# Kernel tuning notes

Measured on AMD Instinct MI355X. Metric: run time of the kernel, lower is better.

The kernel has to match this reference:

```python
import jax, jax.numpy as jnp
import numpy as np

# Per-type input feature dims (NODE_DIM values); max dim = 128 = padded width of x.
NODE_DIMS = np.array([16, 32, 64, 128, 64, 32, 16, 128], dtype=np.int32)
N_TYPES = 8
MAX_DIM = 128
FEAT = 256          # node_feature_dim
N_GRAPHS = 100000   # batch_size; one node of each type per graph


def setup_inputs() -> dict:
    key = jax.random.key(0)
    k1, k2, k3 = jax.random.split(key, 3)
    num_nodes = N_GRAPHS * N_TYPES
    x = jax.random.normal(k1, (num_nodes, MAX_DIM), dtype=jnp.float32)
    # Per-type Linear weights, padded to MAX_DIM on the input axis.
    W = jax.random.normal(k2, (N_TYPES, FEAT, MAX_DIM), dtype=jnp.float32) * 0.05
    b = jax.random.normal(k3, (N_TYPES, FEAT), dtype=jnp.float32) * 0.05
    return {"x": x, "W": W, "b": b}


def reference(x, W, b):
    # Node n = g*N_TYPES + k is the type-k node of graph g (the gather index
    # ptr[b] + node_name.index(k) in the original). Dropout is eval-mode (identity).
    # Mask weight columns beyond each type's true input dim: equivalent to
    # slicing x[:, :NODE_DIM[k]] before the per-type Linear.
    mask = (jnp.arange(MAX_DIM)[None, None, :] < jnp.asarray(NODE_DIMS)[:, None, None]).astype(x.dtype)  # [T,1,D]
    W_eff = W * mask  # [T,F,D]
    xg = x.reshape(N_GRAPHS, N_TYPES, MAX_DIM)  # [G,T,D]
    y = jnp.einsum("gtd,tfd->gtf", xg, W_eff) + b[None, :, :]  # [G,T,F]
    return y.reshape(N_GRAPHS * N_TYPES, FEAT)
```

## Files before the change

kernel.cpp:

```cpp
#include <hip/hip_runtime.h>

#define N_GRAPHS 100000
#define NTYPES 8
#define MAXD 128
#define FEAT 256
#define SPB 8
#define GPB (16 * SPB)

typedef __attribute__((ext_vector_type(8))) short short8;
typedef __attribute__((ext_vector_type(4))) float f32x4;
typedef __attribute__((ext_vector_type(4))) unsigned uint4v;

constexpr int KSN[NTYPES]   = {1, 1, 2, 4, 2, 1, 1, 4};
constexpr int KSOFF[NTYPES] = {0, 1, 2, 4, 8, 10, 11, 12};
constexpr int OFFC[NTYPES]  = {0, 32, 64, 128, 256, 320, 352, 384};
#define KTOT 16
#define LDA 524

__device__ __forceinline__ unsigned f2bf_u(float f) {
    unsigned u = __builtin_bit_cast(unsigned, f);
    return (u + 0x7fffu + ((u >> 16) & 1u)) >> 16;
}
__device__ __forceinline__ unsigned cvt2(float lo, float hi) {
    return f2bf_u(lo) | (f2bf_u(hi) << 16);
}
__device__ __forceinline__ short8 cvt8(f32x4 a, f32x4 b) {
    uint4v u;
    u.x = cvt2(a.x, a.y); u.y = cvt2(a.z, a.w);
    u.z = cvt2(b.x, b.y); u.w = cvt2(b.z, b.w);
    return __builtin_bit_cast(short8, u);
}

__global__ __launch_bounds__(256)
void prepack_w(const float* __restrict__ W, short8* __restrict__ wp)
{
    const int idx  = blockIdx.x * 256 + threadIdx.x;
    const int c16  = idx & 15;
    const int cgrp = (idx >> 4) & 3;
    const int ks   = (idx >> 6) & 3;
    const int ct   = (idx >> 8) & 15;
    const int t    = (idx >> 12) & 7;
    const int col  = ct * 16 + c16;
    const int k    = ks * 32 + cgrp * 8;
    const int dim  = 16 << ((0x30123210u >> (4 * t)) & 0xf);
    const float* src = W + ((size_t)t * FEAT + col) * MAXD + k;
    f32x4 a = *(const f32x4*)src;
    f32x4 b = *(const f32x4*)(src + 4);
    #pragma unroll
    for (int j = 0; j < 4; ++j) {
        if (k + j     >= dim) a[j] = 0.f;
        if (k + 4 + j >= dim) b[j] = 0.f;
    }
    wp[idx] = cvt8(a, b);
}

__device__ __forceinline__ void stage16(const float* __restrict__ x, int gs,
                                        unsigned short (* __restrict__ As)[LDA], int tid)
{
    const int row = tid >> 6;
    const int c8  = tid & 63;
    const int t = (c8 >= 4) + (c8 >= 8) + (c8 >= 16) + (c8 >= 32) +
                  (c8 >= 40) + (c8 >= 44) + (c8 >= 48);
    const int off8 = c8 < 4 ? 0 : c8 < 8 ? 4 : c8 < 16 ? 8 : c8 < 32 ? 16 :
                     c8 < 40 ? 32 : c8 < 44 ? 40 : c8 < 48 ? 44 : 48;
    const int k8 = c8 - off8;
    const float* rp = x + (((size_t)(gs + row)) * NTYPES + t) * MAXD + k8 * 8;
    f32x4 v0 = __builtin_nontemporal_load((const f32x4*)rp);
    f32x4 v1 = __builtin_nontemporal_load((const f32x4*)rp + 1);
    *(short8*)&As[row][c8 * 8] = cvt8(v0, v1);
}

template<int T, bool PRE>
__device__ __forceinline__ void load_bf(short8* __restrict__ Bf,
                                        const short8* __restrict__ wp,
                                        const float* __restrict__ W,
                                        int wave, int cgrp, int c16)
{
    if constexpr (PRE) {
        #pragma unroll
        for (int ks = 0; ks < KSN[T]; ++ks)
            Bf[KSOFF[T] + ks] = wp[(((T * 16 + wave) * 4 + ks) * 4 + cgrp) * 16 + c16];
    } else {
        constexpr int DIM = (T==0||T==6) ? 16 : (T==1||T==5) ? 32 : (T==2||T==4) ? 64 : 128;
        const int col = wave * 16 + c16;
        #pragma unroll
        for (int ks = 0; ks < KSN[T]; ++ks) {
            const int k = ks * 32 + cgrp * 8;
            const float* wf = W + ((size_t)T * FEAT + col) * MAXD + k;
            f32x4 a = *(const f32x4*)wf;
            f32x4 b = *(const f32x4*)(wf + 4);
            #pragma unroll
            for (int j = 0; j < 4; ++j) {
                if (k + j     >= DIM) a[j] = 0.f;
                if (k + 4 + j >= DIM) b[j] = 0.f;
            }
            Bf[KSOFF[T] + ks] = cvt8(a, b);
        }
    }
    if constexpr (T + 1 < NTYPES) load_bf<T + 1, PRE>(Bf, wp, W, wave, cgrp, c16);
}

template<int T>
__device__ __forceinline__ void compute_types(const short8* __restrict__ Bf,
                                              const unsigned short (* __restrict__ A)[LDA],
                                              float* __restrict__ out,
                                              const float* __restrict__ bias_g,
                                              int gs, int wave, int cgrp, int c16)
{
    f32x4 acc = {0.f, 0.f, 0.f, 0.f};
    #pragma unroll
    for (int ks = 0; ks < KSN[T]; ++ks) {
        short8 a = *(const short8*)&A[c16][OFFC[T] + ks * 32 + cgrp * 8];
        acc = __builtin_amdgcn_mfma_f32_16x16x32_bf16(a, Bf[KSOFF[T] + ks], acc, 0, 0, 0);
    }
    const int col = wave * 16 + c16;
    const float bv = bias_g[T * FEAT + col];
    #pragma unroll
    for (int r = 0; r < 4; ++r) {
        const int g = gs + cgrp * 4 + r;
        __builtin_nontemporal_store(acc[r] + bv,
            &out[((size_t)g * NTYPES + T) * FEAT + col]);
    }
    if constexpr (T + 1 < NTYPES) compute_types<T + 1>(Bf, A, out, bias_g, gs, wave, cgrp, c16);
}

template<bool PRE>
__global__ __launch_bounds__(1024, 4)
void node_enc(const float* __restrict__ x, const short8* __restrict__ wp,
              const float* __restrict__ W, const float* __restrict__ bias_g,
              float* __restrict__ out)
{
    __shared__ __align__(16) unsigned short As[2][16][LDA];
    const int tid  = threadIdx.x;
    const int lane = tid & 63;
    const int wave = tid >> 6;
    const int cgrp = lane >> 4;
    const int c16  = lane & 15;
    const int g0   = blockIdx.x * GPB;

    short8 Bf[KTOT];
    load_bf<0, PRE>(Bf, wp, W, wave, cgrp, c16);

    stage16(x, g0, As[0], tid);

    for (int s = 0; s < SPB; ++s) {
        const int gs = g0 + s * 16;
        if (gs >= N_GRAPHS) break;
        __syncthreads();
        const int gn = gs + 16;
        if (s + 1 < SPB && gn < N_GRAPHS)
            stage16(x, gn, As[(s + 1) & 1], tid);
        compute_types<0>(Bf, As[s & 1], out, bias_g, gs, wave, cgrp, c16);
    }
}

extern "C" void kernel_launch(void* const* d_in, const int* in_sizes, int n_in,
                              void* d_out, int out_size, void* d_ws, size_t ws_size,
                              hipStream_t stream)
{
    const float* x = (const float*)d_in[0];
    const float* W = (const float*)d_in[1];
    const float* b = (const float*)d_in[2];
    float* out = (float*)d_out;

    const int grid = (N_GRAPHS + GPB - 1) / GPB;
    const size_t wp_bytes = (size_t)32768 * sizeof(short8);

    if (ws_size >= wp_bytes) {
        short8* wp = (short8*)d_ws;
        prepack_w<<<128, 256, 0, stream>>>(W, wp);
        node_enc<true><<<grid, 1024, 0, stream>>>(x, wp, W, b, out);
    } else {
        node_enc<false><<<grid, 1024, 0, stream>>>(x, nullptr, W, b, out);
    }
}
```

Before: 328.0 us.

## Use persistent 256-thread blocks with 4 column tiles per wave and per-step weight reloads

Replaces the 1024-thread blocks (one 16-column tile per wave, weights held in registers across all steps) with a fixed grid of 768 blocks of 256 threads. Each block covers a contiguous range of graphs and each wave computes four 16-column tiles, which reuses each A fragment across four MFMAs. Weights and bias are now reloaded from the prepacked buffer (L2) for every type on every step instead of staying resident, and each thread stages four rows of x. A tail path with clamped loads and guarded stores handles ranges that are not multiples of 16. This trades register-resident weights for more MFMA work per A load and fewer, persistent blocks, at the cost of repeated weight loads.

```diff
diff --git a/kernel.cpp b/kernel.cpp
--- a/kernel.cpp
+++ b/kernel.cpp
@@ -4,18 +4,15 @@
 #define NTYPES 8
 #define MAXD 128
 #define FEAT 256
-#define SPB 8
-#define GPB (16 * SPB)
+#define NBLK 768
+#define LDA 524
 
 typedef __attribute__((ext_vector_type(8))) short short8;
 typedef __attribute__((ext_vector_type(4))) float f32x4;
 typedef __attribute__((ext_vector_type(4))) unsigned uint4v;
 
-constexpr int KSN[NTYPES]   = {1, 1, 2, 4, 2, 1, 1, 4};
-constexpr int KSOFF[NTYPES] = {0, 1, 2, 4, 8, 10, 11, 12};
-constexpr int OFFC[NTYPES]  = {0, 32, 64, 128, 256, 320, 352, 384};
-#define KTOT 16
-#define LDA 524
+constexpr int KSN[NTYPES]  = {1, 1, 2, 4, 2, 1, 1, 4};
+constexpr int OFFC[NTYPES] = {0, 32, 64, 128, 256, 320, 352, 384};
 
 __device__ __forceinline__ unsigned f2bf_u(float f) {
     unsigned u = __builtin_bit_cast(unsigned, f);
@@ -57,75 +54,93 @@
 __device__ __forceinline__ void stage16(const float* __restrict__ x, int gs,
                                         unsigned short (* __restrict__ As)[LDA], int tid)
 {
-    const int row = tid >> 6;
-    const int c8  = tid & 63;
+    const int c8 = tid & 63;
     const int t = (c8 >= 4) + (c8 >= 8) + (c8 >= 16) + (c8 >= 32) +
                   (c8 >= 40) + (c8 >= 44) + (c8 >= 48);
     const int off8 = c8 < 4 ? 0 : c8 < 8 ? 4 : c8 < 16 ? 8 : c8 < 32 ? 16 :
                      c8 < 40 ? 32 : c8 < 44 ? 40 : c8 < 48 ? 44 : 48;
     const int k8 = c8 - off8;
-    const float* rp = x + (((size_t)(gs + row)) * NTYPES + t) * MAXD + k8 * 8;
-    f32x4 v0 = __builtin_nontemporal_load((const f32x4*)rp);
-    f32x4 v1 = __builtin_nontemporal_load((const f32x4*)rp + 1);
-    *(short8*)&As[row][c8 * 8] = cvt8(v0, v1);
+    #pragma unroll
+    for (int p = 0; p < 4; ++p) {
+        const int row = p * 4 + (tid >> 6);
+        int g = gs + row;
+        if (g > N_GRAPHS - 1) g = N_GRAPHS - 1;
+        const float* rp = x + ((size_t)g * NTYPES + t) * MAXD + k8 * 8;
+        f32x4 v0 = __builtin_nontemporal_load((const f32x4*)rp);
+        f32x4 v1 = __builtin_nontemporal_load((const f32x4*)rp + 1);
+        *(short8*)&As[row][c8 * 8] = cvt8(v0, v1);
+    }
 }
 
-template<int T, bool PRE>
-__device__ __forceinline__ void load_bf(short8* __restrict__ Bf,
-                                        const short8* __restrict__ wp,
-                                        const float* __restrict__ W,
-                                        int wave, int cgrp, int c16)
+template<int T, bool PRE, bool FULL>
+__device__ __forceinline__ void compute_types(const short8* __restrict__ wp,
+                                              const float* __restrict__ W,
+                                              const float* __restrict__ bias_g,
+                                              const unsigned short (* __restrict__ A)[LDA],
+                                              float* __restrict__ out,
+                                              int gs, int gend,
+                                              int wave, int cgrp, int c16)
 {
-    if constexpr (PRE) {
-        #pragma unroll
-        for (int ks = 0; ks < KSN[T]; ++ks)
-            Bf[KSOFF[T] + ks] = wp[(((T * 16 + wave) * 4 + ks) * 4 + cgrp) * 16 + c16];
-    } else {
-        constexpr int DIM = (T==0||T==6) ? 16 : (T==1||T==5) ? 32 : (T==2||T==4) ? 64 : 128;
-        const int col = wave * 16 + c16;
-        #pragma unroll
-        for (int ks = 0; ks < KSN[T]; ++ks) {
-            const int k = ks * 32 + cgrp * 8;
-            const float* wf = W + ((size_t)T * FEAT + col) * MAXD + k;
-            f32x4 a = *(const f32x4*)wf;
-            f32x4 b = *(const f32x4*)(wf + 4);
+    constexpr int KS = KSN[T];
+    short8 Bf[KS][4];
+    float  bias[4];
+    #pragma unroll
+    for (int nt = 0; nt < 4; ++nt) {
+        bias[nt] = bias_g[T * FEAT + wave * 64 + nt * 16 + c16];
+        if constexpr (PRE) {
             #pragma unroll
-            for (int j = 0; j < 4; ++j) {
-                if (k + j     >= DIM) a[j] = 0.f;
-                if (k + 4 + j >= DIM) b[j] = 0.f;
+            for (int ks = 0; ks < KS; ++ks)
+                Bf[ks][nt] = wp[(((T * 16 + wave * 4 + nt) * 4 + ks) * 4 + cgrp) * 16 + c16];
+        } else {
+            constexpr int DIM = (T==0||T==6) ? 16 : (T==1||T==5) ? 32 : (T==2||T==4) ? 64 : 128;
+            const int col = wave * 64 + nt * 16 + c16;
+            #pragma unroll
+            for (int ks = 0; ks < KS; ++ks) {
+                const int k = ks * 32 + cgrp * 8;
+                const float* wf = W + ((size_t)T * FEAT + col) * MAXD + k;
+                f32x4 a = *(const f32x4*)wf;
+                f32x4 b = *(const f32x4*)(wf + 4);
+                #pragma unroll
+                for (int j = 0; j < 4; ++j) {
+                    if (k + j     >= DIM) a[j] = 0.f;
+                    if (k + 4 + j >= DIM) b[j] = 0.f;
+                }
+                Bf[ks][nt] = cvt8(a, b);
             }
-            Bf[KSOFF[T] + ks] = cvt8(a, b);
         }
     }
-    if constexpr (T + 1 < NTYPES) load_bf<T + 1, PRE>(Bf, wp, W, wave, cgrp, c16);
-}
 
-template<int T>
-__device__ __forceinline__ void compute_types(const short8* __restrict__ Bf,
-                                              const unsigned short (* __restrict__ A)[LDA],
-                                              float* __restrict__ out,
-                                              const float* __restrict__ bias_g,
-                                              int gs, int wave, int cgrp, int c16)
-{
-    f32x4 acc = {0.f, 0.f, 0.f, 0.f};
+    short8 a[KS];
     #pragma unroll
-    for (int ks = 0; ks < KSN[T]; ++ks) {
-        short8 a = *(const short8*)&A[c16][OFFC[T] + ks * 32 + cgrp * 8];
-        acc = __builtin_amdgcn_mfma_f32_16x16x32_bf16(a, Bf[KSOFF[T] + ks], acc, 0, 0, 0);
+    for (int ks = 0; ks < KS; ++ks)
+        a[ks] = *(const short8*)&A[c16][OFFC[T] + ks * 32 + cgrp * 8];
+
+    f32x4 acc[4] = {{0,0,0,0},{0,0,0,0},{0,0,0,0},{0,0,0,0}};
+    #pragma unroll
+    for (int ks = 0; ks < KS; ++ks) {
+        #pragma unroll
+        for (int nt = 0; nt < 4; ++nt)
+            acc[nt] = __builtin_amdgcn_mfma_f32_16x16x32_bf16(a[ks], Bf[ks][nt], acc[nt], 0, 0, 0);
     }
-    const int col = wave * 16 + c16;
-    const float bv = bias_g[T * FEAT + col];
+
     #pragma unroll
-    for (int r = 0; r < 4; ++r) {
-        const int g = gs + cgrp * 4 + r;
-        __builtin_nontemporal_store(acc[r] + bv,
-            &out[((size_t)g * NTYPES + T) * FEAT + col]);
+    for (int nt = 0; nt < 4; ++nt) {
+        const int col = wave * 64 + nt * 16 + c16;
+        #pragma unroll
+        for (int r = 0; r < 4; ++r) {
+            const int g = gs + cgrp * 4 + r;
+            if (FULL || g < gend)
+                __builtin_nontemporal_store(acc[nt][r] + bias[nt],
+                    &out[((size_t)g * NTYPES + T) * FEAT + col]);
+        }
     }
-    if constexpr (T + 1 < NTYPES) compute_types<T + 1>(Bf, A, out, bias_g, gs, wave, cgrp, c16);
+
+    if constexpr (T + 1 < NTYPES)
+        compute_types<T + 1, PRE, FULL>(wp, W, bias_g, A, out, gs, gend, wave, cgrp, c16);
 }
 
 template<bool PRE>
-__global__ __launch_bounds__(1024, 4)
+__global__ __launch_bounds__(256, 3)
 void node_enc(const float* __restrict__ x, const short8* __restrict__ wp,
               const float* __restrict__ W, const float* __restrict__ bias_g,
               float* __restrict__ out)
@@ -136,21 +151,22 @@
     const int wave = tid >> 6;
     const int cgrp = lane >> 4;
     const int c16  = lane & 15;
-    const int g0   = blockIdx.x * GPB;
+    const long long b = blockIdx.x;
+    const int gstart = (int)(b * N_GRAPHS / NBLK);
+    const int gend   = (int)((b + 1) * N_GRAPHS / NBLK);
+    const int ns     = (gend - gstart + 15) >> 4;
 
-    short8 Bf[KTOT];
-    load_bf<0, PRE>(Bf, wp, W, wave, cgrp, c16);
+    stage16(x, gstart, As[0], tid);
 
-    stage16(x, g0, As[0], tid);
-
-    for (int s = 0; s < SPB; ++s) {
-        const int gs = g0 + s * 16;
-        if (gs >= N_GRAPHS) break;
+    for (int s = 0; s < ns; ++s) {
+        asm volatile("" ::: "memory");
         __syncthreads();
-        const int gn = gs + 16;
-        if (s + 1 < SPB && gn < N_GRAPHS)
-            stage16(x, gn, As[(s + 1) & 1], tid);
-        compute_types<0>(Bf, As[s & 1], out, bias_g, gs, wave, cgrp, c16);
+        const int gs = gstart + s * 16;
+        if (s + 1 < ns) stage16(x, gs + 16, As[(s + 1) & 1], tid);
+        if (gs + 16 <= gend)
+            compute_types<0, PRE, true >(wp, W, bias_g, As[s & 1], out, gs, gend, wave, cgrp, c16);
+        else
+            compute_types<0, PRE, false>(wp, W, bias_g, As[s & 1], out, gs, gend, wave, cgrp, c16);
     }
 }
 
@@ -163,14 +179,13 @@
     const float* b = (const float*)d_in[2];
     float* out = (float*)d_out;
 
-    const int grid = (N_GRAPHS + GPB - 1) / GPB;
     const size_t wp_bytes = (size_t)32768 * sizeof(short8);
 
     if (ws_size >= wp_bytes) {
         short8* wp = (short8*)d_ws;
         prepack_w<<<128, 256, 0, stream>>>(W, wp);
-        node_enc<true><<<grid, 1024, 0, stream>>>(x, wp, W, b, out);
+        node_enc<true><<<NBLK, 256, 0, stream>>>(x, wp, W, b, out);
     } else {
-        node_enc<false><<<grid, 1024, 0, stream>>>(x, nullptr, W, b, out);
+        node_enc<false><<<NBLK, 256, 0, stream>>>(x, nullptr, W, b, out);
     }
 }
```

Measured after the change: 411.1 us. 1.25x slower.
